# Performance work log

Measured on AMD Instinct MI355X. Metric: run time of the kernel, lower is better.

The kernel has to match this reference:

```python
import jax, jax.numpy as jnp
import numpy as np

GAMMA = 1.0  # RBF kernel width (init kwarg gamma)
N_PAIRS = 8_388_608
N_LAYERS = 8


def setup_inputs() -> dict:
    key = jax.random.key(0)
    ks = jax.random.split(key, 12)
    inp = {
        "x": jax.random.normal(ks[0], (N_PAIRS, 2), dtype=jnp.float32),
        "y": jax.random.normal(ks[1], (N_PAIRS, 2), dtype=jnp.float32),
        # input layer (clip=False)
        "W0": jax.random.normal(ks[2], (2, 2), dtype=jnp.float32),
        "b0": jax.random.normal(ks[3], (2,), dtype=jnp.float32),
        "scale0": jax.random.uniform(ks[4], (2,), dtype=jnp.float32),
        "shift0": jax.random.normal(ks[5], (2,), dtype=jnp.float32),
        # hidden layers (weights/biases clipped to [-5, 5] at construction)
        "Ws": jnp.clip(jax.random.normal(ks[6], (N_LAYERS, 2, 2), dtype=jnp.float32), -5.0, 5.0),
        "bs": jnp.clip(jax.random.normal(ks[7], (N_LAYERS, 2), dtype=jnp.float32), -5.0, 5.0),
        "scales": jax.random.uniform(ks[8], (N_LAYERS, 2), dtype=jnp.float32),
        "shifts": jax.random.normal(ks[9], (N_LAYERS, 2), dtype=jnp.float32),
        # final head Linear(2, 1)
        "Wf": jax.random.normal(ks[10], (1, 2), dtype=jnp.float32),
        "bf": jax.random.normal(ks[11], (1,), dtype=jnp.float32),
    }
    return inp


def _fraud_net(z, W0, b0, scale0, shift0, Ws, bs, scales, shifts, Wf, bf):
    # input layer: tanh(Linear(2,2)) * scale + shift   (z: [N,2])
    z = jnp.tanh(z @ W0.T + b0) * scale0 + shift0

    def step(z, p):
        W, b, s, t = p
        return jnp.tanh(z @ W.T + b) * s + t, None

    z, _ = jax.lax.scan(step, z, (Ws, bs, scales, shifts))
    # final Linear(2, 1) then squeeze -> [N]
    return (z @ Wf.T + bf)[..., 0]


def reference(x, y, W0, b0, scale0, shift0, Ws, bs, scales, shifts, Wf, bf):
    diff = x - y  # [N, 2]
    rbf = jnp.exp(-GAMMA * jnp.sum(diff * diff, axis=-1))  # [N]
    fx = _fraud_net(x, W0, b0, scale0, shift0, Ws, bs, scales, shifts, Wf, bf)
    fy = _fraud_net(y, W0, b0, scale0, shift0, Ws, bs, scales, shifts, Wf, bf)
    return rbf * fx * fy  # [N]
```

## Files before the change

### kernel.cpp

```cpp
#include <hip/hip_runtime.h>
#include <math.h>

#define N_LAYERS 8
#define TAB 64
#define TABSZ (TAB * TAB)
#define LOG2E2 2.8853900817779268f
#define NLOG2E 1.4426950408889634f
#define UCLAMP 24.0f

#if __has_builtin(__builtin_amdgcn_exp2f)
__device__ __forceinline__ float exp2_fast(float x) { return __builtin_amdgcn_exp2f(x); }
#else
__device__ __forceinline__ float exp2_fast(float x) { return __expf(0.6931471805599453f * x); }
#endif

__global__ void setup_meta(const float* __restrict__ W0, const float* __restrict__ b0,
                           const float* __restrict__ s0, const float* __restrict__ t0,
                           float* __restrict__ fp) {
    if (threadIdx.x == 0 && blockIdx.x == 0) {
        fp[0] = LOG2E2 * W0[0]; fp[1] = LOG2E2 * W0[1];
        fp[2] = LOG2E2 * W0[2]; fp[3] = LOG2E2 * W0[3];
        fp[4] = LOG2E2 * b0[0]; fp[5] = LOG2E2 * b0[1];
        for (int c = 0; c < 2; ++c) {
            float s = s0[c], t = t0[c];
            float span = fmaxf(2.2f * s, 1e-5f);
            float h  = span / (float)(TAB - 1);
            float lo = t - 0.5f * span;
            float ih = (float)(TAB - 1) / span;
            fp[6 + c]  = (s + 0.5f * span) * ih;
            fp[8 + c]  = 2.0f * s * ih;
            fp[10 + c] = lo;
            fp[12 + c] = h;
        }
    }
}

__global__ void build_table(const float* __restrict__ Ws, const float* __restrict__ bs,
                            const float* __restrict__ ss, const float* __restrict__ ts,
                            const float* __restrict__ Wf, const float* __restrict__ bf,
                            const float* __restrict__ fp, float* __restrict__ gt) {
    int idx = blockIdx.x * 256 + threadIdx.x;
    if (idx >= TABSZ) return;
    int k0 = idx & (TAB - 1);
    int k1 = idx >> 6;
    float z0 = fp[10] + (float)k0 * fp[12];
    float z1 = fp[11] + (float)k1 * fp[13];
    for (int l = 0; l < N_LAYERS; ++l) {
        float u0 = fmaf(z0, Ws[4 * l + 0], fmaf(z1, Ws[4 * l + 1], bs[2 * l + 0]));
        float u1 = fmaf(z0, Ws[4 * l + 2], fmaf(z1, Ws[4 * l + 3], bs[2 * l + 1]));
        z0 = fmaf(tanhf(u0), ss[2 * l + 0], ts[2 * l + 0]);
        z1 = fmaf(tanhf(u1), ss[2 * l + 1], ts[2 * l + 1]);
    }
    gt[idx] = fmaf(z0, Wf[0], fmaf(z1, Wf[1], bf[0]));
}

__device__ __forceinline__ void cr_w(float f, float w[4]) {
    w[0] = f * fmaf(f, fmaf(f, -0.5f, 1.0f), -0.5f);
    w[1] = fmaf(f * f, fmaf(f, 1.5f, -2.5f), 1.0f);
    w[2] = f * fmaf(f, fmaf(f, -1.5f, 2.0f), 0.5f);
    w[3] = f * f * fmaf(f, 0.5f, -0.5f);
}

__device__ __forceinline__ float interp2d(const float* __restrict__ tab, float u0, float u1) {
    int ix = (int)u0, iy = (int)u1;
    ix = min(max(ix, 1), TAB - 3);
    iy = min(max(iy, 1), TAB - 3);
    float fx = u0 - (float)ix, fy = u1 - (float)iy;
    float wx[4], wy[4];
    cr_w(fx, wx);
    cr_w(fy, wy);
    const float* p = tab + (iy - 1) * TAB + (ix - 1);
    float r0 = fmaf(p[3], wx[3], fmaf(p[2], wx[2], fmaf(p[1], wx[1], p[0] * wx[0]))); p += TAB;
    float r1 = fmaf(p[3], wx[3], fmaf(p[2], wx[2], fmaf(p[1], wx[1], p[0] * wx[0]))); p += TAB;
    float r2 = fmaf(p[3], wx[3], fmaf(p[2], wx[2], fmaf(p[1], wx[1], p[0] * wx[0]))); p += TAB;
    float r3 = fmaf(p[3], wx[3], fmaf(p[2], wx[2], fmaf(p[1], wx[1], p[0] * wx[0])));
    return fmaf(r3, wy[3], fmaf(r2, wy[2], fmaf(r1, wy[1], r0 * wy[0])));
}

__device__ __forceinline__ float pair_val(const float* __restrict__ tab,
                                          float px0, float px1, float py0, float py1,
                                          float C0, float C1, float D0, float D1) {
    float d0 = exp2_fast(fminf(px0, UCLAMP)) + 1.0f;
    float d1 = exp2_fast(fminf(px1, UCLAMP)) + 1.0f;
    float d2 = exp2_fast(fminf(py0, UCLAMP)) + 1.0f;
    float d3 = exp2_fast(fminf(py1, UCLAMP)) + 1.0f;
    float p2 = d0 * d1, p3 = p2 * d2, p4 = p3 * d3;
    float R = __builtin_amdgcn_rcpf(p4);
    float i3 = R * p3;  R *= d3;
    float i2 = R * p2;  R *= d2;
    float i1 = R * d0;
    float i0 = R * d1;
    float ux0 = fmaf(-D0, i0, C0), ux1 = fmaf(-D1, i1, C1);
    float uy0 = fmaf(-D0, i2, C0), uy1 = fmaf(-D1, i3, C1);
    return interp2d(tab, ux0, ux1) * interp2d(tab, uy0, uy1);
}

__global__ __launch_bounds__(256, 4) void fraud_kernel(
    const float4* __restrict__ x4, const float4* __restrict__ y4,
    const float* __restrict__ fp, const float* __restrict__ gt,
    float2* __restrict__ out2, int stride)
{
    __shared__ float tab[TABSZ];
    {
        const float4* g4 = (const float4*)gt;
        float4* t4 = (float4*)tab;
        for (int j = threadIdx.x; j < TABSZ / 4; j += 256) t4[j] = g4[j];
    }
    __syncthreads();

    float Wt0 = fp[0], Wt1 = fp[1], Wt2 = fp[2], Wt3 = fp[3];
    float bt0 = fp[4], bt1 = fp[5];
    float C0 = fp[6], C1 = fp[7], D0 = fp[8], D1 = fp[9];

    int tid = blockIdx.x * 256 + threadIdx.x;
#pragma unroll
    for (int k = 0; k < 4; ++k) {
        int g = tid + k * stride;
        float4 xa = x4[g], ya = y4[g];

        float pxa0 = fmaf(xa.x, Wt0, fmaf(xa.y, Wt1, bt0));
        float pxa1 = fmaf(xa.x, Wt2, fmaf(xa.y, Wt3, bt1));
        float pya0 = fmaf(ya.x, Wt0, fmaf(ya.y, Wt1, bt0));
        float pya1 = fmaf(ya.x, Wt2, fmaf(ya.y, Wt3, bt1));
        float dxA = xa.x - ya.x, dyA = xa.y - ya.y;
        float rA = exp2_fast(-NLOG2E * fmaf(dxA, dxA, dyA * dyA));
        float resA = rA * pair_val(tab, pxa0, pxa1, pya0, pya1, C0, C1, D0, D1);

        float pxb0 = fmaf(xa.z, Wt0, fmaf(xa.w, Wt1, bt0));
        float pxb1 = fmaf(xa.z, Wt2, fmaf(xa.w, Wt3, bt1));
        float pyb0 = fmaf(ya.z, Wt0, fmaf(ya.w, Wt1, bt0));
        float pyb1 = fmaf(ya.z, Wt2, fmaf(ya.w, Wt3, bt1));
        float dxB = xa.z - ya.z, dyB = xa.w - ya.w;
        float rB = exp2_fast(-NLOG2E * fmaf(dxB, dxB, dyB * dyB));
        float resB = rB * pair_val(tab, pxb0, pxb1, pyb0, pyb1, C0, C1, D0, D1);

        out2[g] = make_float2(resA, resB);
    }
}

extern "C" void kernel_launch(void* const* d_in, const int* in_sizes, int n_in,
                              void* d_out, int out_size, void* d_ws, size_t ws_size,
                              hipStream_t stream) {
    const float* x  = (const float*)d_in[0];
    const float* y  = (const float*)d_in[1];
    const float* W0 = (const float*)d_in[2];
    const float* b0 = (const float*)d_in[3];
    const float* s0 = (const float*)d_in[4];
    const float* t0 = (const float*)d_in[5];
    const float* Ws = (const float*)d_in[6];
    const float* bs = (const float*)d_in[7];
    const float* ss = (const float*)d_in[8];
    const float* ts = (const float*)d_in[9];
    const float* Wf = (const float*)d_in[10];
    const float* bf = (const float*)d_in[11];
    float* out = (float*)d_out;
    float* fp  = (float*)d_ws;
    float* gt  = fp + 16;

    hipLaunchKernelGGL(setup_meta, dim3(1), dim3(64), 0, stream, W0, b0, s0, t0, fp);
    hipLaunchKernelGGL(build_table, dim3(TABSZ / 256), dim3(256), 0, stream,
                       Ws, bs, ss, ts, Wf, bf, fp, gt);

    int n       = out_size;
    int ngroups = n / 2;
    int threads = ngroups / 4;
    dim3 block(256);
    dim3 grid(threads / 256);
    hipLaunchKernelGGL(fraud_kernel, grid, block, 0, stream,
                       (const float4*)x, (const float4*)y, fp, gt,
                       (float2*)out, threads);
}
```

Baseline: 199.7 us.

## Pack interpolation table as float4 stencils and shrink table to 48x48

Adds a pack_table kernel that stores, for each table cell, the four horizontal Catmull-Rom neighbours as one float4. The main kernel can then fetch each stencil row with a single 128-bit LDS read instead of four scalar reads. The table shrinks from 64x64 to 48x48 so the 4x-expanded copy (36 KB of LDS per block) stays manageable. The occupancy hint of 4 blocks per CU is dropped from launch bounds. The trade-offs are lower interpolation accuracy, a larger per-block shared-memory fill from global, and one extra tiny kernel launch.

Result: faster. 193.9 us (-2.9%).

```diff
diff --git a/kernel.cpp b/kernel.cpp
--- a/kernel.cpp
+++ b/kernel.cpp
@@ -2,7 +2,7 @@
 #include <math.h>
 
 #define N_LAYERS 8
-#define TAB 64
+#define TAB 48
 #define TABSZ (TAB * TAB)
 #define LOG2E2 2.8853900817779268f
 #define NLOG2E 1.4426950408889634f
@@ -41,8 +41,7 @@
                             const float* __restrict__ fp, float* __restrict__ gt) {
     int idx = blockIdx.x * 256 + threadIdx.x;
     if (idx >= TABSZ) return;
-    int k0 = idx & (TAB - 1);
-    int k1 = idx >> 6;
+    int k1 = idx / TAB, k0 = idx - k1 * TAB;
     float z0 = fp[10] + (float)k0 * fp[12];
     float z1 = fp[11] + (float)k1 * fp[13];
     for (int l = 0; l < N_LAYERS; ++l) {
@@ -54,6 +53,18 @@
     gt[idx] = fmaf(z0, Wf[0], fmaf(z1, Wf[1], bf[0]));
 }
 
+__global__ void pack_table(const float* __restrict__ gt, float4* __restrict__ gt4) {
+    int idx = blockIdx.x * 256 + threadIdx.x;
+    if (idx >= TABSZ) return;
+    int iy = idx / TAB, ix = idx - iy * TAB;
+    const float* row = gt + iy * TAB;
+    int c0 = max(ix - 1, 0);
+    int c1 = ix;
+    int c2 = min(ix + 1, TAB - 1);
+    int c3 = min(ix + 2, TAB - 1);
+    gt4[idx] = make_float4(row[c0], row[c1], row[c2], row[c3]);
+}
+
 __device__ __forceinline__ void cr_w(float f, float w[4]) {
     w[0] = f * fmaf(f, fmaf(f, -0.5f, 1.0f), -0.5f);
     w[1] = fmaf(f * f, fmaf(f, 1.5f, -2.5f), 1.0f);
@@ -61,23 +72,40 @@
     w[3] = f * f * fmaf(f, 0.5f, -0.5f);
 }
 
-__device__ __forceinline__ float interp2d(const float* __restrict__ tab, float u0, float u1) {
-    int ix = (int)u0, iy = (int)u1;
-    ix = min(max(ix, 1), TAB - 3);
-    iy = min(max(iy, 1), TAB - 3);
-    float fx = u0 - (float)ix, fy = u1 - (float)iy;
-    float wx[4], wy[4];
-    cr_w(fx, wx);
-    cr_w(fy, wy);
-    const float* p = tab + (iy - 1) * TAB + (ix - 1);
-    float r0 = fmaf(p[3], wx[3], fmaf(p[2], wx[2], fmaf(p[1], wx[1], p[0] * wx[0]))); p += TAB;
-    float r1 = fmaf(p[3], wx[3], fmaf(p[2], wx[2], fmaf(p[1], wx[1], p[0] * wx[0]))); p += TAB;
-    float r2 = fmaf(p[3], wx[3], fmaf(p[2], wx[2], fmaf(p[1], wx[1], p[0] * wx[0]))); p += TAB;
-    float r3 = fmaf(p[3], wx[3], fmaf(p[2], wx[2], fmaf(p[1], wx[1], p[0] * wx[0])));
-    return fmaf(r3, wy[3], fmaf(r2, wy[2], fmaf(r1, wy[1], r0 * wy[0])));
+__device__ __forceinline__ float interp_two(const float4* __restrict__ tab4,
+                                            float ax0, float ax1, float ay0, float ay1) {
+    int ixa = min(max((int)ax0, 1), TAB - 3);
+    int iya = min(max((int)ax1, 1), TAB - 3);
+    int ixb = min(max((int)ay0, 1), TAB - 3);
+    int iyb = min(max((int)ay1, 1), TAB - 3);
+    float fxa = ax0 - (float)ixa, fya = ax1 - (float)iya;
+    float fxb = ay0 - (float)ixb, fyb = ay1 - (float)iyb;
+
+    const float4* pa = tab4 + (iya - 1) * TAB + ixa;
+    const float4* pb = tab4 + (iyb - 1) * TAB + ixb;
+    float4 a0 = pa[0], a1 = pa[TAB], a2 = pa[2 * TAB], a3 = pa[3 * TAB];
+    float4 b0 = pb[0], b1 = pb[TAB], b2 = pb[2 * TAB], b3 = pb[3 * TAB];
+
+    float wxa[4], wya[4], wxb[4], wyb[4];
+    cr_w(fxa, wxa); cr_w(fya, wya);
+    cr_w(fxb, wxb); cr_w(fyb, wyb);
+
+    float ra0 = fmaf(a0.w, wxa[3], fmaf(a0.z, wxa[2], fmaf(a0.y, wxa[1], a0.x * wxa[0])));
+    float ra1 = fmaf(a1.w, wxa[3], fmaf(a1.z, wxa[2], fmaf(a1.y, wxa[1], a1.x * wxa[0])));
+    float ra2 = fmaf(a2.w, wxa[3], fmaf(a2.z, wxa[2], fmaf(a2.y, wxa[1], a2.x * wxa[0])));
+    float ra3 = fmaf(a3.w, wxa[3], fmaf(a3.z, wxa[2], fmaf(a3.y, wxa[1], a3.x * wxa[0])));
+    float gx  = fmaf(ra3, wya[3], fmaf(ra2, wya[2], fmaf(ra1, wya[1], ra0 * wya[0])));
+
+    float rb0 = fmaf(b0.w, wxb[3], fmaf(b0.z, wxb[2], fmaf(b0.y, wxb[1], b0.x * wxb[0])));
+    float rb1 = fmaf(b1.w, wxb[3], fmaf(b1.z, wxb[2], fmaf(b1.y, wxb[1], b1.x * wxb[0])));
+    float rb2 = fmaf(b2.w, wxb[3], fmaf(b2.z, wxb[2], fmaf(b2.y, wxb[1], b2.x * wxb[0])));
+    float rb3 = fmaf(b3.w, wxb[3], fmaf(b3.z, wxb[2], fmaf(b3.y, wxb[1], b3.x * wxb[0])));
+    float gy  = fmaf(rb3, wyb[3], fmaf(rb2, wyb[2], fmaf(rb1, wyb[1], rb0 * wyb[0])));
+
+    return gx * gy;
 }
 
-__device__ __forceinline__ float pair_val(const float* __restrict__ tab,
+__device__ __forceinline__ float pair_val(const float4* __restrict__ tab4,
                                           float px0, float px1, float py0, float py1,
                                           float C0, float C1, float D0, float D1) {
     float d0 = exp2_fast(fminf(px0, UCLAMP)) + 1.0f;
@@ -92,20 +120,16 @@
     float i0 = R * d1;
     float ux0 = fmaf(-D0, i0, C0), ux1 = fmaf(-D1, i1, C1);
     float uy0 = fmaf(-D0, i2, C0), uy1 = fmaf(-D1, i3, C1);
-    return interp2d(tab, ux0, ux1) * interp2d(tab, uy0, uy1);
+    return interp_two(tab4, ux0, ux1, uy0, uy1);
 }
 
-__global__ __launch_bounds__(256, 4) void fraud_kernel(
+__global__ __launch_bounds__(256) void fraud_kernel(
     const float4* __restrict__ x4, const float4* __restrict__ y4,
-    const float* __restrict__ fp, const float* __restrict__ gt,
+    const float* __restrict__ fp, const float4* __restrict__ gt4,
     float2* __restrict__ out2, int stride)
 {
-    __shared__ float tab[TABSZ];
-    {
-        const float4* g4 = (const float4*)gt;
-        float4* t4 = (float4*)tab;
-        for (int j = threadIdx.x; j < TABSZ / 4; j += 256) t4[j] = g4[j];
-    }
+    __shared__ float4 tab4[TABSZ];
+    for (int j = threadIdx.x; j < TABSZ; j += 256) tab4[j] = gt4[j];
     __syncthreads();
 
     float Wt0 = fp[0], Wt1 = fp[1], Wt2 = fp[2], Wt3 = fp[3];
@@ -124,7 +148,7 @@
         float pya1 = fmaf(ya.x, Wt2, fmaf(ya.y, Wt3, bt1));
         float dxA = xa.x - ya.x, dyA = xa.y - ya.y;
         float rA = exp2_fast(-NLOG2E * fmaf(dxA, dxA, dyA * dyA));
-        float resA = rA * pair_val(tab, pxa0, pxa1, pya0, pya1, C0, C1, D0, D1);
+        float resA = rA * pair_val(tab4, pxa0, pxa1, pya0, pya1, C0, C1, D0, D1);
 
         float pxb0 = fmaf(xa.z, Wt0, fmaf(xa.w, Wt1, bt0));
         float pxb1 = fmaf(xa.z, Wt2, fmaf(xa.w, Wt3, bt1));
@@ -132,7 +156,7 @@
         float pyb1 = fmaf(ya.z, Wt2, fmaf(ya.w, Wt3, bt1));
         float dxB = xa.z - ya.z, dyB = xa.w - ya.w;
         float rB = exp2_fast(-NLOG2E * fmaf(dxB, dxB, dyB * dyB));
-        float resB = rB * pair_val(tab, pxb0, pxb1, pyb0, pyb1, C0, C1, D0, D1);
+        float resB = rB * pair_val(tab4, pxb0, pxb1, pyb0, pyb1, C0, C1, D0, D1);
 
         out2[g] = make_float2(resA, resB);
     }
@@ -156,10 +180,13 @@
     float* out = (float*)d_out;
     float* fp  = (float*)d_ws;
     float* gt  = fp + 16;
+    float4* gt4 = (float4*)(fp + 16 + TABSZ);
 
     hipLaunchKernelGGL(setup_meta, dim3(1), dim3(64), 0, stream, W0, b0, s0, t0, fp);
-    hipLaunchKernelGGL(build_table, dim3(TABSZ / 256), dim3(256), 0, stream,
+    hipLaunchKernelGGL(build_table, dim3((TABSZ + 255) / 256), dim3(256), 0, stream,
                        Ws, bs, ss, ts, Wf, bf, fp, gt);
+    hipLaunchKernelGGL(pack_table, dim3((TABSZ + 255) / 256), dim3(256), 0, stream,
+                       gt, gt4);
 
     int n       = out_size;
     int ngroups = n / 2;
@@ -167,6 +194,6 @@
     dim3 block(256);
     dim3 grid(threads / 256);
     hipLaunchKernelGGL(fraud_kernel, grid, block, 0, stream,
-                       (const float4*)x, (const float4*)y, fp, gt,
+                       (const float4*)x, (const float4*)y, fp, gt4,
                        (float2*)out, threads);
 }
```
